# Performance work log

Measured on AMD Instinct MI355X. Metric: run time of the kernel, lower is better.

Reference implementation:

```python
import jax, jax.numpy as jnp
import numpy as np

N = 512    # nnodes
H = 8      # attention heads
C = 32     # gnn_repr_size (per head)
ER = 32    # edge_repr_size
FE = 3     # feat_emb_size
E = 16384  # edges (avg degree 32)


def gat_conv(x, edge_index, edge_attr, W, att_src, att_dst, We, att_edge, b):
    """PyG GATConv (edge_dim=1, concat=True, add_self_loops=True, eval mode)."""
    n = x.shape[0]
    h_, c_ = att_src.shape
    row, col = edge_index[0], edge_index[1]
    # self loops with fill_value='mean': mean of incoming edge_attr per target node
    deg = jax.ops.segment_sum(jnp.ones_like(edge_attr), col, num_segments=n)
    loop_attr = jax.ops.segment_sum(edge_attr, col, num_segments=n) / jnp.maximum(deg, 1.0)
    ar = jnp.arange(n)
    row = jnp.concatenate([row, ar])
    col = jnp.concatenate([col, ar])
    ea = jnp.concatenate([edge_attr, loop_attr])
    # node projections [n, H, C]
    h = (x @ W.T).reshape(n, h_, c_)
    a_src = jnp.sum(h * att_src, axis=-1)  # [n, H]
    a_dst = jnp.sum(h * att_dst, axis=-1)  # [n, H]
    e = (ea[:, None] @ We.T).reshape(-1, h_, c_)  # [E', H, C]
    a_e = jnp.sum(e * att_edge, axis=-1)          # [E', H]
    alpha = jax.nn.leaky_relu(a_src[row] + a_dst[col] + a_e, 0.2)
    # softmax over edges grouped by destination node
    amax = jax.ops.segment_max(alpha, col, num_segments=n)
    ex = jnp.exp(alpha - amax[col])
    denom = jax.ops.segment_sum(ex, col, num_segments=n)
    alpha = ex / (denom[col] + 1e-16)
    out = jax.ops.segment_sum(h[row] * alpha[..., None], col, num_segments=n)
    return out.reshape(n, h_ * c_) + b


def setup_inputs():
    key = jax.random.key(0)
    ks = jax.random.split(key, 24)
    s = 0.05
    HC = H * C
    in_len = N * ER + 3 * N + 3 * FE  # combiner1 input length
    return {
        "dist": jax.random.uniform(ks[0], (N, N), dtype=jnp.float32),
        "markov": jax.random.uniform(ks[1], (N, N), dtype=jnp.float32),
        "demand": jax.random.normal(ks[2], (N,), dtype=jnp.float32),
        "W_week": jax.random.normal(ks[3], (7, FE)) * s,
        "W_cap": jax.random.normal(ks[4], (26, FE)) * s,
        "W_veh": jax.random.normal(ks[5], (15, FE)) * s,
        "g1_W": jax.random.normal(ks[6], (HC, 1)) * s,
        "g1_att_src": jax.random.normal(ks[7], (H, C)) * s,
        "g1_att_dst": jax.random.normal(ks[8], (H, C)) * s,
        "g1_We": jax.random.normal(ks[9], (HC, 1)) * s,
        "g1_att_edge": jax.random.normal(ks[10], (H, C)) * s,
        "g1_b": jnp.zeros((HC,), dtype=jnp.float32),
        "g2_W": jax.random.normal(ks[11], (HC, HC)) * s,
        "g2_att_src": jax.random.normal(ks[12], (H, C)) * s,
        "g2_att_dst": jax.random.normal(ks[13], (H, C)) * s,
        "g2_We": jax.random.normal(ks[14], (HC, 1)) * s,
        "g2_att_edge": jax.random.normal(ks[15], (H, C)) * s,
        "g2_b": jnp.zeros((HC,), dtype=jnp.float32),
        "Wes": jax.random.normal(ks[16], (ER, 2 * HC)) * s,
        "bes": jnp.zeros((ER,), dtype=jnp.float32),
        "Wc1": jax.random.normal(ks[17], (N, in_len)) * 0.01,
        "bc1": jnp.zeros((N,), dtype=jnp.float32),
        "Wc2": jax.random.normal(ks[18], (N, N)) * s,
        "bc2": jnp.zeros((N,), dtype=jnp.float32),
        "stops": jax.random.randint(ks[19], (256,), 0, N),
        "edge_index": jax.random.randint(ks[20], (2, E), 0, N),
        "weekday": 3,
        "vehicles": 7,
        "capacity": 12,
    }


def reference(dist, markov, demand, W_week, W_cap, W_veh,
              g1_W, g1_att_src, g1_att_dst, g1_We, g1_att_edge, g1_b,
              g2_W, g2_att_src, g2_att_dst, g2_We, g2_att_edge, g2_b,
              Wes, bes, Wc1, bc1, Wc2, bc2,
              stops, edge_index, weekday, vehicles, capacity):
    n = dist.shape[0]
    dist = (dist - dist.min()) / (dist.max() - dist.min())
    x = demand[:, None]  # [n, 1]
    ea = markov[edge_index[0], edge_index[1]]  # [E]
    x = jax.nn.relu(gat_conv(x, edge_index, ea, g1_W, g1_att_src, g1_att_dst, g1_We, g1_att_edge, g1_b))
    x = jax.nn.relu(gat_conv(x, edge_index, ea, g2_W, g2_att_src, g2_att_dst, g2_We, g2_att_edge, g2_b))
    HC_ = x.shape[1]
    # all-pairs edge representation: concat(x[i], x[j]) over meshgrid -> [n*n, 2*HC]
    er = jnp.concatenate([
        jnp.broadcast_to(x[:, None, :], (n, n, HC_)),
        jnp.broadcast_to(x[None, :, :], (n, n, HC_)),
    ], axis=-1).reshape(n * n, 2 * HC_)
    er = (er @ Wes.T + bes).reshape(n, -1)  # [n, n*ER]
    week = jnp.broadcast_to(W_week[weekday], (n, W_week.shape[1]))
    cap = jnp.broadcast_to(W_cap[capacity], (n, W_cap.shape[1]))
    veh = jnp.broadcast_to(W_veh[vehicles], (n, W_veh.shape[1]))
    stop = jnp.broadcast_to(jnp.zeros((n,), dtype=dist.dtype).at[stops].set(1.0)[None, :], (n, n))
    feat = jnp.concatenate([er, dist, markov, week, cap, veh, stop], axis=1)
    out = jax.nn.relu(feat @ Wc1.T + bc1) @ Wc2.T + bc2
    return out
```

## Files before the change

kernel.cpp:

```cpp
#include <hip/hip_runtime.h>
#include <hip/hip_bf16.h>

typedef __hip_bfloat16 bf16;
typedef __attribute__((ext_vector_type(8))) short bf16x8;
typedef __attribute__((ext_vector_type(4))) float f32x4;

#define NNODE 512
#define NEDGE 16384
#define INLEN 17929
#define K1P   1088

#define WS_EA      0
#define WS_CSRC    16384
#define WS_CEA     32768
#define WS_DEG     49152
#define WS_STARTS  49664
#define WS_LATTR   50176
#define WS_MM      50688
#define WS_MMP     50690
#define WS_STOPV   50818
#define WS_AE      51330
#define WS_PS      51346
#define WS_G2WT    186624
#define WS_Y       317696
#define WS_ASRC    448768
#define WS_ADST    452864
#define WS_UV      456960
#define WS_K       489728
#define WS_APACK   490240
#define WS_BPACK   768768
#define WS_X1      1047296
#define WS_WC2B    1178368
#define WS_WESF    1309440
#define WS_ASRC2   1325824
#define WS_ADST2   1329920
#define WS_CURSOR  1334016
#define WS_DEGP    1334528
#define WS_LSUMP   1367296
#define WS_OUT1F   1400064

static __device__ __forceinline__ unsigned short f2bfbits(float x){
  bf16 b = __float2bfloat16(x);
  union { bf16 b; unsigned short u; } c; c.b = b; return c.u;
}

__global__ __launch_bounds__(256)
void k_prep(const float* __restrict__ demand, const float* __restrict__ W1,
            const float* __restrict__ att_s, const float* __restrict__ att_d,
            const int* __restrict__ stops, const float* __restrict__ Wes,
            const float* __restrict__ dist, const float* __restrict__ markov,
            const int* __restrict__ eidx,
            const float* __restrict__ g1We, const float* __restrict__ g1ae,
            const float* __restrict__ g2We, const float* __restrict__ g2ae,
            const float* __restrict__ g2W,  const float* __restrict__ g2as,
            const float* __restrict__ g2ad, const float* __restrict__ Wc2,
            float* __restrict__ outp, float* ws){
  int b = blockIdx.x, tid = threadIdx.x;
  if (b < 512){
    int hd = tid>>5, c = tid&31;
    float hv = demand[b] * W1[tid];
    float ps = hv * att_s[tid];
    float pd = hv * att_d[tid];
    for (int off=16; off; off>>=1){ ps += __shfl_down(ps,off,32); pd += __shfl_down(pd,off,32); }
    if (c==0){ ws[WS_ASRC + b*8+hd]=ps; ws[WS_ADST + b*8+hd]=pd; }
  } else if (b == 512){
    ws[WS_STOPV+tid] = 0.f; ws[WS_STOPV+256+tid] = 0.f;
    __syncthreads();
    ws[WS_STOPV + stops[tid]] = 1.0f;
    if (tid < 8){
      float s=0.f; for (int c=0;c<32;c++) s += g1We[tid*32+c]*g1ae[tid*32+c];
      ws[WS_AE+tid]=s;
    } else if (tid < 16){
      int h=tid-8; float s=0.f; for (int c=0;c<32;c++) s += g2We[h*32+c]*g2ae[h*32+c];
      ws[WS_AE+8+h]=s;
    }
  } else if (b < 515){
    for (int idx = (b-513)*8192 + tid; idx < (b-512)*8192; idx += 256){
      int k = idx>>8, c = idx&255;
      ws[WS_WESF+idx] = (k<32) ? Wes[k*512+c] : Wes[(k-32)*512+256+c];
    }
  } else if (b < 579){
    __shared__ float smn[256], smx[256];
    int p = b-515;
    float mn = 3.4e38f, mx = -3.4e38f;
    const float4* dv = (const float4*)(dist + p*4096);
    #pragma unroll
    for (int k=0;k<4;k++){
      float4 v = dv[k*256 + tid];
      mn = fminf(mn, fminf(fminf(v.x,v.y), fminf(v.z,v.w)));
      mx = fmaxf(mx, fmaxf(fmaxf(v.x,v.y), fmaxf(v.z,v.w)));
    }
    smn[tid]=mn; smx[tid]=mx; __syncthreads();
    for (int off=128; off; off>>=1){
      if (tid<off){ smn[tid]=fminf(smn[tid],smn[tid+off]); smx[tid]=fmaxf(smx[tid],smx[tid+off]); }
      __syncthreads();
    }
    if (tid==0){ ws[WS_MMP+p]=smn[0]; ws[WS_MMP+64+p]=smx[0]; }
  } else if (b < 643){
    __shared__ int   hd_[512];
    __shared__ float hf_[512];
    int k = b-579;
    hd_[tid]=0; hd_[256+tid]=0; hf_[tid]=0.f; hf_[256+tid]=0.f;
    __syncthreads();
    int e = k*256 + tid;
    int r = eidx[e], c = eidx[NEDGE+e];
    float a = markov[r*NNODE + c];
    ws[WS_EA+e] = a;
    atomicAdd(&hd_[c], 1);
    atomicAdd(&hf_[c], a);
    __syncthreads();
    ((int*)(ws+WS_DEGP))[k*512+tid]     = hd_[tid];
    ((int*)(ws+WS_DEGP))[k*512+256+tid] = hd_[256+tid];
    ws[WS_LSUMP + k*512+tid]     = hf_[tid];
    ws[WS_LSUMP + k*512+256+tid] = hf_[256+tid];
  } else if (b < 659){
    int j = b-643;
    const float* att = (j<8) ? g2as : g2ad;
    int h = j&7;
    float s = 0.f;
    for (int c=0;c<32;c++) s += att[h*32+c] * g2W[(h*32+c)*256 + tid];
    ws[WS_PS + j*256 + tid] = s;
  } else if (b < 675){
    __shared__ float T[64][65];
    int tb = b-659, tr = tb>>2, tc = tb&3;
    int w = tid>>6, c = tid&63;
    for (int k=0;k<16;k++){
      int r = k*4 + w;
      T[r][c] = g2W[(tr*64+r)*256 + tc*64 + c];
    }
    __syncthreads();
    for (int k=0;k<16;k++){
      int r = k*4 + w;
      ws[WS_G2WT + (tc*64+r)*256 + tr*64 + c] = T[c][r];
    }
  } else if (b == 675){
    ((int*)(ws+WS_CURSOR))[tid] = 0;
    ((int*)(ws+WS_CURSOR))[256+tid] = 0;
  } else if (b < 740){
    int blk = b - 676;
    const float4* src = (const float4*)(Wc2 + blk*4096);
    ushort4* dst = (ushort4*)((unsigned short*)(ws+WS_WC2B) + blk*4096);
    #pragma unroll
    for (int i=0;i<4;i++){
      float4 v = src[i*256+tid];
      ushort4 u;
      u.x = f2bfbits(v.x); u.y = f2bfbits(v.y);
      u.z = f2bfbits(v.z); u.w = f2bfbits(v.w);
      dst[i*256+tid] = u;
    }
  } else {
    int blk = b - 740;
    float4 z = {0.f,0.f,0.f,0.f};
    float4* o1f = (float4*)(ws + WS_OUT1F);
    float4* op  = (float4*)outp;
    o1f[blk*512 + tid] = z;
    o1f[blk*512 + 256 + tid] = z;
    op[blk*512 + tid] = z;
    op[blk*512 + 256 + tid] = z;
  }
}

__global__ __launch_bounds__(512)
void k_scansc(const int* __restrict__ eidx, float* ws){
  __shared__ int startS[512];
  __shared__ int wsum[8];
  int t = threadIdx.x, b = blockIdx.x, lane = t&63, w = t>>6;
  const int* dp = (const int*)(ws+WS_DEGP);
  int d = 0;
  #pragma unroll 8
  for (int k=0;k<64;k++) d += dp[k*512+t];
  int v = d;
  for (int off=1; off<64; off<<=1){
    int u = __shfl_up(v, off, 64);
    if (lane >= off) v += u;
  }
  if (lane==63) wsum[w] = v;
  __syncthreads();
  int base = 0;
  for (int k=0;k<w;k++) base += wsum[k];
  int incl = base + v;
  startS[t] = incl - d;
  if (b == 0){
    float l = 0.f;
    for (int k=0;k<64;k++) l += ws[WS_LSUMP+k*512+t];
    ((int*)(ws+WS_STARTS))[t] = incl - d;
    ((int*)(ws+WS_DEG))[t] = d;
    ws[WS_LATTR+t] = l / (float)(d>1 ? d : 1);
    if (t < 64){
      float mn = ws[WS_MMP+t], mx = ws[WS_MMP+64+t];
      for (int off=32; off; off>>=1){
        mn = fminf(mn, __shfl_down(mn,off,64));
        mx = fmaxf(mx, __shfl_down(mx,off,64));
      }
      if (t==0){ ws[WS_MM]=mn; ws[WS_MM+1]=mx; }
    }
  }
  __syncthreads();
  int e = b*512 + t;
  int c = eidx[NEDGE+e];
  int p = startS[c] + atomicAdd((int*)(ws+WS_CURSOR)+c, 1);
  ((int*)(ws+WS_CSRC))[p] = eidx[e];
  ws[WS_CEA+p] = ws[WS_EA+e];
}

template<int MODE>
__global__ __launch_bounds__(256)
void k_agg(const float* __restrict__ asrc, const float* __restrict__ adst,
           const float* __restrict__ AEp, const float* __restrict__ demand,
           const float* __restrict__ w1, const float* __restrict__ b1,
           float* ws){
  int t = blockIdx.x, tid = threadIdx.x, hd = tid>>5;
  __shared__ int   srcE[256];
  __shared__ float eaE[256];
  __shared__ float demE[256];
  __shared__ float Lall[256*8];
  __shared__ float AE[8], mh[8], dh[8], sw[8], sagg[8];
  __shared__ float xrow[256];
  if (tid<8) AE[tid]=AEp[tid];
  __syncthreads();
  const int* csrc = (const int*)(ws+WS_CSRC);
  const float* cea = ws+WS_CEA;
  int d  = ((const int*)(ws+WS_DEG))[t];
  int s0 = ((const int*)(ws+WS_STARTS))[t];
  if (d > 256) d = 256;
  for (int e=tid; e<d; e+=256){
    int s = csrc[s0+e];
    srcE[e]=s; eaE[e]=cea[s0+e];
    if (MODE==1) demE[e]=demand[s];
  }
  __syncthreads();
  {
    int h8 = tid&7;
    float adt = adst[t*8+h8], aeh = AE[h8];
    for (int e = tid>>3; e < d; e += 32){
      float a = asrc[srcE[e]*8+h8] + adt + eaE[e]*aeh;
      Lall[e*8+h8] = a>=0.f ? a : 0.2f*a;
    }
  }
  __syncthreads();
  {
    int h = tid>>5, j = tid&31;
    float aself = asrc[t*8+h] + adst[t*8+h] + ws[WS_LATTR+t]*AE[h];
    aself = aself>=0.f ? aself : 0.2f*aself;
    float mm = aself;
    for (int e=j; e<d; e+=32) mm = fmaxf(mm, Lall[e*8+h]);
    for (int off=16; off; off>>=1) mm = fmaxf(mm, __shfl_down(mm,off,32));
    mm = __shfl(mm, 0, 32);
    float dd = 0.f;
    for (int e=j; e<d; e+=32) dd += __expf(Lall[e*8+h]-mm);
    for (int off=16; off; off>>=1) dd += __shfl_down(dd,off,32);
    if (j==0){
      float se = __expf(aself-mm);
      mh[h]=mm; dh[h]=dd+se+1e-16f; sw[h]=se;
    }
  }
  __syncthreads();
  {
    int h8 = tid&7;
    for (int e = tid>>3; e < d; e += 32)
      Lall[e*8+h8] = __expf(Lall[e*8+h8] - mh[h8]);
  }
  __syncthreads();
  if (MODE == 1){
    int h = tid>>5, j = tid&31;
    float s = 0.f;
    for (int e=j; e<d; e+=32) s += Lall[e*8+h]*demE[e];
    for (int off=16; off; off>>=1) s += __shfl_down(s,off,32);
    if (j==0) sagg[h] = (s + sw[h]*demand[t]) / dh[h];
    __syncthreads();
    float v = fmaxf(sagg[hd]*w1[tid] + b1[tid], 0.f);
    xrow[tid] = v;
    ws[WS_X1 + t*256 + tid] = v;
    __syncthreads();
    if (tid < 64){
      int j2 = tid>>2, q = tid&3;
      const float* pr = ws + WS_PS + j2*256 + q*64;
      const float* xr = xrow + q*64;
      float p = 0.f;
      for (int c=0;c<64;c++) p += xr[c]*pr[c];
      p += __shfl_down(p,2,4);
      p += __shfl_down(p,1,4);
      if (q==0){
        if (j2<8) ws[WS_ASRC2 + t*8+j2] = p;
        else      ws[WS_ADST2 + t*8+(j2-8)] = p;
      }
    }
  } else {
    const float* x1 = ws + WS_X1;
    float a0 = sw[hd]*x1[t*256+tid], a1=0.f, a2=0.f, a3=0.f, a4=0.f, a5=0.f, a6=0.f, a7=0.f;
    int e = 0;
    for (; e+8<=d; e+=8){
      a0 += Lall[(e+0)*8+hd]*x1[srcE[e+0]*256+tid];
      a1 += Lall[(e+1)*8+hd]*x1[srcE[e+1]*256+tid];
      a2 += Lall[(e+2)*8+hd]*x1[srcE[e+2]*256+tid];
      a3 += Lall[(e+3)*8+hd]*x1[srcE[e+3]*256+tid];
      a4 += Lall[(e+4)*8+hd]*x1[srcE[e+4]*256+tid];
      a5 += Lall[(e+5)*8+hd]*x1[srcE[e+5]*256+tid];
      a6 += Lall[(e+6)*8+hd]*x1[srcE[e+6]*256+tid];
      a7 += Lall[(e+7)*8+hd]*x1[srcE[e+7]*256+tid];
    }
    for (; e<d; e++) a0 += Lall[e*8+hd]*x1[srcE[e]*256+tid];
    ws[WS_Y + t*256 + tid] = (((a0+a1)+(a2+a3))+((a4+a5)+(a6+a7)))/dh[hd];
  }
}

__global__ __launch_bounds__(256)
void k_post(const float* __restrict__ dist, const float* __restrict__ markov,
            const float* __restrict__ g2b, float* ws){
  __shared__ float yls[4][256];
  __shared__ float o2[4][256];
  __shared__ float uvs[4][64];
  int b = blockIdx.x, tid = threadIdx.x, n0 = b*4;
  #pragma unroll
  for (int n=0;n<4;n++) yls[n][tid] = ws[WS_Y + (n0+n)*256 + tid];
  __syncthreads();
  const float* T = ws + WS_G2WT;
  float a0=0.f,a1=0.f,a2=0.f,a3=0.f;
  #pragma unroll 4
  for (int c=0;c<256;c++){
    float w = T[c*256+tid];
    a0 += yls[0][c]*w; a1 += yls[1][c]*w;
    a2 += yls[2][c]*w; a3 += yls[3][c]*w;
  }
  float bb = g2b[tid];
  o2[0][tid]=fmaxf(a0+bb,0.f); o2[1][tid]=fmaxf(a1+bb,0.f);
  o2[2][tid]=fmaxf(a2+bb,0.f); o2[3][tid]=fmaxf(a3+bb,0.f);
  __syncthreads();
  {
    int n = tid>>6, k = tid&63;
    const float* wk = ws + WS_WESF + k*256;
    float p = 0.f;
    #pragma unroll 4
    for (int c=0;c<256;c++) p += o2[n][c]*wk[c];
    uvs[n][k] = p;
    ws[WS_UV + (n0+n)*64 + k] = p;
  }
  __syncthreads();
  float mn = ws[WS_MM], mx = ws[WS_MM+1];
  float inv = 1.0f/(mx-mn);
  bf16* ap = (bf16*)(ws+WS_APACK);
  #pragma unroll
  for (int n=0;n<4;n++){
    int t = n0+n;
    const float* drow = dist + t*512;
    const float* mrow = markov + t*512;
    for (int j=tid; j<K1P; j+=256){
      float v2;
      if (j<32)        v2 = uvs[n][j];
      else if (j<544)  v2 = (drow[j-32] - mn) * inv;
      else if (j<1056) v2 = mrow[j-544];
      else             v2 = 0.f;
      ap[(size_t)t*K1P + j] = __float2bfloat16(v2);
    }
  }
}

__global__ __launch_bounds__(1024)
void k_skpack(const float* __restrict__ Wc1, const float* __restrict__ bc1,
              const float* __restrict__ bes, const float* __restrict__ Wweek,
              const float* __restrict__ Wcap, const float* __restrict__ Wveh,
              const int* __restrict__ wd, const int* __restrict__ vh,
              const int* __restrict__ cp, float* ws){
  int o = blockIdx.x, tid = threadIdx.x;
  __shared__ float besf[32];
  __shared__ float red[512];
  __shared__ float red2[16];
  if (tid<32) besf[tid] = bes[tid];
  __syncthreads();
  const float* wr = Wc1 + (size_t)o*INLEN;
  bf16* bp  = (bf16*)(ws+WS_BPACK);
  float be = besf[tid&31];
  const float* uvp = ws + WS_UV + ((tid>>5)<<6) + 32 + (tid&31);
  float sP = 0.f, tP0=0.f, tP1=0.f, tP2=0.f, tP3=0.f;
  #pragma unroll
  for (int i=0;i<16;i+=4){
    float w0 = wr[tid + 1024*(i+0)];
    float w1 = wr[tid + 1024*(i+1)];
    float w2 = wr[tid + 1024*(i+2)];
    float w3 = wr[tid + 1024*(i+3)];
    float u0 = uvp[2048*(i+0)];
    float u1 = uvp[2048*(i+1)];
    float u2 = uvp[2048*(i+2)];
    float u3 = uvp[2048*(i+3)];
    sP += (w0+w1)+(w2+w3);
    tP0 += w0*(u0+be);
    tP1 += w1*(u1+be);
    tP2 += w2*(u2+be);
    tP3 += w3*(u3+be);
  }
  float tP = (tP0+tP1)+(tP2+tP3);
  if (tid < 512) tP += ws[WS_STOPV+tid] * wr[17417+tid];
  if (tid < 9){
    int g = tid/3, f = tid-g*3;
    float sv = (g==0) ? Wweek[wd[0]*3+f]
             : (g==1) ? Wcap[cp[0]*3+f]
                      : Wveh[vh[0]*3+f];
    tP += sv * wr[17408+tid];
  }
  int lane = tid&63, w = tid>>6;
  sP += __shfl_down(sP, 32, 64);
  if (lane < 32) red[w*32 + lane] = sP;
  for (int off=32; off; off>>=1) tP += __shfl_down(tP, off, 64);
  if (lane == 0) red2[w] = tP;
  __syncthreads();
  if (tid < 32){
    float s = 0.f;
    #pragma unroll
    for (int k=0;k<16;k++) s += red[k*32+tid];
    bp[(size_t)o*K1P + tid] = __float2bfloat16(s);
    bp[(size_t)o*K1P + 1056 + tid] = __float2bfloat16(0.f);
  } else if (tid == 32){
    float s = 0.f;
    #pragma unroll
    for (int k=0;k<16;k++) s += red2[k];
    ws[WS_K+o] = s + bc1[o];
  }
  bp[(size_t)o*K1P + 32 + tid] = __float2bfloat16(wr[16384+tid]);
}

__global__ __launch_bounds__(512)
void gemm1_splitk(const bf16* __restrict__ A, const bf16* __restrict__ B,
                  float* __restrict__ C, int N, int K){
  __shared__ short Als[2][4096];
  __shared__ short Bls[2][4096];
  const int tid = threadIdx.x;
  const int bm = blockIdx.y*64, bn = blockIdx.x*64;
  const int kz = blockIdx.z, NS = gridDim.z;
  const int nkT = K>>6;
  const int kb = (nkT*kz)/NS, ke = (nkT*(kz+1))/NS, cnt = ke-kb;
  const int wave = tid>>6, lane = tid&63;
  const int wm = wave>>2, wn = wave&3;
  const int r = lane&15, q = lane>>4;
  f32x4 acc[2] = {};
  const int lrow = tid>>3, lk8 = tid&7;
  const bf16* Ag = A + (size_t)(bm+lrow)*K + kb*64 + lk8*8;
  const bf16* Bg = B + (size_t)(bn+lrow)*K + kb*64 + lk8*8;
  const int sidx = ((lk8>>2)*256 + (lk8&3)*64 + lrow)*8;
  float4 av = *(const float4*)(Ag);
  float4 bv = *(const float4*)(Bg);
  *(float4*)(&Als[0][sidx]) = av;
  *(float4*)(&Bls[0][sidx]) = bv;
  __syncthreads();
  for (int kk=0; kk<cnt; kk++){
    int cur = kk&1, nxt = cur^1;
    if (kk+1 < cnt){
      av = *(const float4*)(Ag + (kk+1)*64);
      bv = *(const float4*)(Bg + (kk+1)*64);
    }
    #pragma unroll
    for (int k2=0; k2<2; k2++){
      bf16x8 bfr = *(const bf16x8*)(&Bls[cur][(k2*256 + q*64 + wn*16 + r)*8]);
      #pragma unroll
      for (int i=0;i<2;i++){
        bf16x8 af = *(const bf16x8*)(&Als[cur][(k2*256 + q*64 + wm*32 + i*16 + r)*8]);
        acc[i] = __builtin_amdgcn_mfma_f32_16x16x32_bf16(af, bfr, acc[i], 0,0,0);
      }
    }
    if (kk+1 < cnt){
      __syncthreads();
      *(float4*)(&Als[nxt][sidx]) = av;
      *(float4*)(&Bls[nxt][sidx]) = bv;
      __syncthreads();
    }
  }
  const int col = bn + wn*16 + r;
  #pragma unroll
  for (int i=0;i<2;i++){
    int row = bm + wm*32 + i*16 + q*4;
    #pragma unroll
    for (int g=0; g<4; g++)
      atomicAdd(&C[(size_t)(row+g)*N + col], acc[i][g]);
  }
}

__global__ __launch_bounds__(512)
void gemm2_f32a(const float* __restrict__ Af, const bf16* __restrict__ B,
                const float* __restrict__ kbias, const float* __restrict__ bc2,
                float* __restrict__ C){
  const int N = 512, K = 512;
  __shared__ short Als[2][4096];
  __shared__ short Bls[2][4096];
  const int tid = threadIdx.x;
  const int bm = blockIdx.y*64, bn = blockIdx.x*64;
  const int kz = blockIdx.z, NS = gridDim.z;
  const int nkT = K>>6;
  const int kb = (nkT*kz)/NS, ke = (nkT*(kz+1))/NS, cnt = ke-kb;
  const int wave = tid>>6, lane = tid&63;
  const int wm = wave>>2, wn = wave&3;
  const int r = lane&15, q = lane>>4;
  f32x4 acc[2] = {};
  const int lrow = tid>>3, lk8 = tid&7;
  const float* Ag = Af + (size_t)(bm+lrow)*K + kb*64 + lk8*8;
  const bf16*  Bg = B  + (size_t)(bn+lrow)*K + kb*64 + lk8*8;
  const float* Kg = kbias + kb*64 + lk8*8;
  const int sidx = ((lk8>>2)*256 + (lk8&3)*64 + lrow)*8;
  union PK { ushort u[8]; float4 f; };
  float4 x0, x1, k0, k1, bv;
  auto loadA = [&](int kk){
    x0 = *(const float4*)(Ag + kk*64);
    x1 = *(const float4*)(Ag + kk*64 + 4);
    k0 = *(const float4*)(Kg + kk*64);
    k1 = *(const float4*)(Kg + kk*64 + 4);
  };
  auto packA = [&]()->float4 {
    PK p;
    p.u[0]=f2bfbits(fmaxf(x0.x+k0.x,0.f));
    p.u[1]=f2bfbits(fmaxf(x0.y+k0.y,0.f));
    p.u[2]=f2bfbits(fmaxf(x0.z+k0.z,0.f));
    p.u[3]=f2bfbits(fmaxf(x0.w+k0.w,0.f));
    p.u[4]=f2bfbits(fmaxf(x1.x+k1.x,0.f));
    p.u[5]=f2bfbits(fmaxf(x1.y+k1.y,0.f));
    p.u[6]=f2bfbits(fmaxf(x1.z+k1.z,0.f));
    p.u[7]=f2bfbits(fmaxf(x1.w+k1.w,0.f));
    return p.f;
  };
  loadA(0);
  bv = *(const float4*)(Bg);
  *(float4*)(&Als[0][sidx]) = packA();
  *(float4*)(&Bls[0][sidx]) = bv;
  __syncthreads();
  for (int kk=0; kk<cnt; kk++){
    int cur = kk&1, nxt = cur^1;
    if (kk+1 < cnt){
      loadA(kk+1);
      bv = *(const float4*)(Bg + (kk+1)*64);
    }
    #pragma unroll
    for (int k2=0; k2<2; k2++){
      bf16x8 bfr = *(const bf16x8*)(&Bls[cur][(k2*256 + q*64 + wn*16 + r)*8]);
      #pragma unroll
      for (int i=0;i<2;i++){
        bf16x8 af = *(const bf16x8*)(&Als[cur][(k2*256 + q*64 + wm*32 + i*16 + r)*8]);
        acc[i] = __builtin_amdgcn_mfma_f32_16x16x32_bf16(af, bfr, acc[i], 0,0,0);
      }
    }
    if (kk+1 < cnt){
      __syncthreads();
      *(float4*)(&Als[nxt][sidx]) = packA();
      *(float4*)(&Bls[nxt][sidx]) = bv;
      __syncthreads();
    }
  }
  const int col = bn + wn*16 + r;
  const float bi = (kz==0) ? bc2[col] : 0.f;
  #pragma unroll
  for (int i=0;i<2;i++){
    int row = bm + wm*32 + i*16 + q*4;
    #pragma unroll
    for (int g=0; g<4; g++)
      atomicAdd(&C[(size_t)(row+g)*N + col], acc[i][g] + bi);
  }
}

extern "C" void kernel_launch(void* const* d_in, const int* in_sizes, int n_in,
                              void* d_out, int out_size, void* d_ws, size_t ws_size,
                              hipStream_t stream){
  const float* dist   = (const float*)d_in[0];
  const float* markov = (const float*)d_in[1];
  const float* demand = (const float*)d_in[2];
  const float* Wweek  = (const float*)d_in[3];
  const float* Wcap   = (const float*)d_in[4];
  const float* Wveh   = (const float*)d_in[5];
  const float* g1W    = (const float*)d_in[6];
  const float* g1as   = (const float*)d_in[7];
  const float* g1ad   = (const float*)d_in[8];
  const float* g1We   = (const float*)d_in[9];
  const float* g1ae   = (const float*)d_in[10];
  const float* g1b    = (const float*)d_in[11];
  const float* g2W    = (const float*)d_in[12];
  const float* g2as   = (const float*)d_in[13];
  const float* g2ad   = (const float*)d_in[14];
  const float* g2We   = (const float*)d_in[15];
  const float* g2ae   = (const float*)d_in[16];
  const float* g2b    = (const float*)d_in[17];
  const float* Wes    = (const float*)d_in[18];
  const float* bes    = (const float*)d_in[19];
  const float* Wc1    = (const float*)d_in[20];
  const float* bc1    = (const float*)d_in[21];
  const float* Wc2    = (const float*)d_in[22];
  const float* bc2    = (const float*)d_in[23];
  const int*   stops  = (const int*)d_in[24];
  const int*   eidx   = (const int*)d_in[25];
  const int*   wd     = (const int*)d_in[26];
  const int*   vh     = (const int*)d_in[27];
  const int*   cp     = (const int*)d_in[28];
  float* out = (float*)d_out;
  float* ws = (float*)d_ws;

  k_prep<<<868,256,0,stream>>>(demand, g1W, g1as, g1ad, stops, Wes, dist, markov, eidx,
                               g1We, g1ae, g2We, g2ae, g2W, g2as, g2ad, Wc2, out, ws);
  k_scansc<<<32,512,0,stream>>>(eidx, ws);
  k_agg<1><<<512,256,0,stream>>>(ws+WS_ASRC, ws+WS_ADST, ws+WS_AE, demand, g1W, g1b, ws);
  k_agg<2><<<512,256,0,stream>>>(ws+WS_ASRC2, ws+WS_ADST2, ws+WS_AE+8, demand, g1W, g1b, ws);
  k_post<<<128,256,0,stream>>>(dist, markov, g2b, ws);
  k_skpack<<<512,1024,0,stream>>>(Wc1, bc1, bes, Wweek, Wcap, Wveh, wd, vh, cp, ws);
  gemm1_splitk<<<dim3(8,8,4),512,0,stream>>>((const bf16*)(ws+WS_APACK), (const bf16*)(ws+WS_BPACK),
                                             ws+WS_OUT1F, 512, K1P);
  gemm2_f32a<<<dim3(8,8,2),512,0,stream>>>(ws+WS_OUT1F, (const bf16*)(ws+WS_WC2B),
                                           ws+WS_K, bc2, out);
}
```

Baseline: 214.7 us.

## Fuse GAT layer-2 projection and post-processing into aggregation kernels

Layer-2's linear projection moves ahead of aggregation: it is computed per node inside the first aggregation kernel (x1·W2ᵀ), so the second aggregation gathers already-projected features. The second aggregation then applies bias and ReLU, computes the edge-repr U/V projection, and packs the GEMM A rows, which removes the separate k_post kernel and the X1/Y round-trips. The transposed g2W and the Wes weights are stored as packed bf16 pairs to halve weight reads, at some cost in precision.

New measurement: 191.4 us. 1.12x faster.

```diff
diff --git a/kernel.cpp b/kernel.cpp
--- a/kernel.cpp
+++ b/kernel.cpp
@@ -22,14 +22,13 @@
 #define WS_AE      51330
 #define WS_PS      51346
 #define WS_G2WT    186624
-#define WS_Y       317696
+#define WS_H2      317696
 #define WS_ASRC    448768
 #define WS_ADST    452864
 #define WS_UV      456960
 #define WS_K       489728
 #define WS_APACK   490240
 #define WS_BPACK   768768
-#define WS_X1      1047296
 #define WS_WC2B    1178368
 #define WS_WESF    1309440
 #define WS_ASRC2   1325824
@@ -75,9 +74,16 @@
       ws[WS_AE+8+h]=s;
     }
   } else if (b < 515){
-    for (int idx = (b-513)*8192 + tid; idx < (b-512)*8192; idx += 256){
-      int k = idx>>8, c = idx&255;
-      ws[WS_WESF+idx] = (k<32) ? Wes[k*512+c] : Wes[(k-32)*512+256+c];
+    unsigned int* wp = (unsigned int*)(ws+WS_WESF);
+    int k0 = (b-513)*32;
+    for (int it=0; it<16; ++it){
+      int idx = it*256 + tid;
+      int k = k0 + (idx>>7), c2 = idx&127;
+      int c = 2*c2;
+      float lo, hi;
+      if (k<32){ lo = Wes[k*512+c];           hi = Wes[k*512+c+1]; }
+      else     { lo = Wes[(k-32)*512+256+c];  hi = Wes[(k-32)*512+256+c+1]; }
+      wp[k*128+c2] = ((unsigned int)f2bfbits(lo)) | (((unsigned int)f2bfbits(hi))<<16);
     }
   } else if (b < 579){
     __shared__ float smn[256], smx[256];
@@ -129,9 +135,13 @@
       T[r][c] = g2W[(tr*64+r)*256 + tc*64 + c];
     }
     __syncthreads();
-    for (int k=0;k<16;k++){
-      int r = k*4 + w;
-      ws[WS_G2WT + (tc*64+r)*256 + tr*64 + c] = T[c][r];
+    unsigned int* gp = (unsigned int*)(ws+WS_G2WT);
+    for (int k=0;k<8;k++){
+      int r0 = k*8 + w*2;
+      float lo = T[c][r0], hi = T[c][r0+1];
+      unsigned int u = ((unsigned int)f2bfbits(lo)) | (((unsigned int)f2bfbits(hi))<<16);
+      int i0 = tc*64 + r0;
+      gp[(i0>>1)*256 + tr*64 + c] = u;
     }
   } else if (b == 675){
     ((int*)(ws+WS_CURSOR))[tid] = 0;
@@ -205,9 +215,11 @@
 
 template<int MODE>
 __global__ __launch_bounds__(256)
-void k_agg(const float* __restrict__ asrc, const float* __restrict__ adst,
-           const float* __restrict__ AEp, const float* __restrict__ demand,
-           const float* __restrict__ w1, const float* __restrict__ b1,
+void k_agg(const float* __restrict__ hbuf, const float* __restrict__ asrc,
+           const float* __restrict__ adst, const float* __restrict__ AEp,
+           const float* __restrict__ bvec, const float* __restrict__ demand,
+           const float* __restrict__ w1,
+           const float* __restrict__ dist, const float* __restrict__ markov,
            float* ws){
   int t = blockIdx.x, tid = threadIdx.x, hd = tid>>5;
   __shared__ int   srcE[256];
@@ -215,7 +227,7 @@
   __shared__ float demE[256];
   __shared__ float Lall[256*8];
   __shared__ float AE[8], mh[8], dh[8], sw[8], sagg[8];
-  __shared__ float xrow[256];
+  __shared__ float xrow[256], uvrow[64];
   if (tid<8) AE[tid]=AEp[tid];
   __syncthreads();
   const int* csrc = (const int*)(ws+WS_CSRC);
@@ -268,10 +280,18 @@
     for (int off=16; off; off>>=1) s += __shfl_down(s,off,32);
     if (j==0) sagg[h] = (s + sw[h]*demand[t]) / dh[h];
     __syncthreads();
-    float v = fmaxf(sagg[hd]*w1[tid] + b1[tid], 0.f);
+    float v = fmaxf(sagg[hd]*w1[tid] + bvec[tid], 0.f);
     xrow[tid] = v;
-    ws[WS_X1 + t*256 + tid] = v;
-    __syncthreads();
+    __syncthreads();
+    const unsigned int* g2 = (const unsigned int*)(ws+WS_G2WT);
+    float h0=0.f, h1=0.f;
+    #pragma unroll 4
+    for (int p=0;p<128;p++){
+      unsigned int wv = g2[p*256+tid];
+      h0 += xrow[2*p]   * __uint_as_float(wv<<16);
+      h1 += xrow[2*p+1] * __uint_as_float(wv & 0xffff0000u);
+    }
+    ws[WS_H2 + t*256 + tid] = h0+h1;
     if (tid < 64){
       int j2 = tid>>2, q = tid&3;
       const float* pr = ws + WS_PS + j2*256 + q*64;
@@ -286,68 +306,45 @@
       }
     }
   } else {
-    const float* x1 = ws + WS_X1;
-    float a0 = sw[hd]*x1[t*256+tid], a1=0.f, a2=0.f, a3=0.f, a4=0.f, a5=0.f, a6=0.f, a7=0.f;
+    float a0 = sw[hd]*hbuf[t*256+tid], a1=0.f, a2=0.f, a3=0.f, a4=0.f, a5=0.f, a6=0.f, a7=0.f;
     int e = 0;
     for (; e+8<=d; e+=8){
-      a0 += Lall[(e+0)*8+hd]*x1[srcE[e+0]*256+tid];
-      a1 += Lall[(e+1)*8+hd]*x1[srcE[e+1]*256+tid];
-      a2 += Lall[(e+2)*8+hd]*x1[srcE[e+2]*256+tid];
-      a3 += Lall[(e+3)*8+hd]*x1[srcE[e+3]*256+tid];
-      a4 += Lall[(e+4)*8+hd]*x1[srcE[e+4]*256+tid];
-      a5 += Lall[(e+5)*8+hd]*x1[srcE[e+5]*256+tid];
-      a6 += Lall[(e+6)*8+hd]*x1[srcE[e+6]*256+tid];
-      a7 += Lall[(e+7)*8+hd]*x1[srcE[e+7]*256+tid];
-    }
-    for (; e<d; e++) a0 += Lall[e*8+hd]*x1[srcE[e]*256+tid];
-    ws[WS_Y + t*256 + tid] = (((a0+a1)+(a2+a3))+((a4+a5)+(a6+a7)))/dh[hd];
-  }
-}
-
-__global__ __launch_bounds__(256)
-void k_post(const float* __restrict__ dist, const float* __restrict__ markov,
-            const float* __restrict__ g2b, float* ws){
-  __shared__ float yls[4][256];
-  __shared__ float o2[4][256];
-  __shared__ float uvs[4][64];
-  int b = blockIdx.x, tid = threadIdx.x, n0 = b*4;
-  #pragma unroll
-  for (int n=0;n<4;n++) yls[n][tid] = ws[WS_Y + (n0+n)*256 + tid];
-  __syncthreads();
-  const float* T = ws + WS_G2WT;
-  float a0=0.f,a1=0.f,a2=0.f,a3=0.f;
-  #pragma unroll 4
-  for (int c=0;c<256;c++){
-    float w = T[c*256+tid];
-    a0 += yls[0][c]*w; a1 += yls[1][c]*w;
-    a2 += yls[2][c]*w; a3 += yls[3][c]*w;
-  }
-  float bb = g2b[tid];
-  o2[0][tid]=fmaxf(a0+bb,0.f); o2[1][tid]=fmaxf(a1+bb,0.f);
-  o2[2][tid]=fmaxf(a2+bb,0.f); o2[3][tid]=fmaxf(a3+bb,0.f);
-  __syncthreads();
-  {
-    int n = tid>>6, k = tid&63;
-    const float* wk = ws + WS_WESF + k*256;
-    float p = 0.f;
-    #pragma unroll 4
-    for (int c=0;c<256;c++) p += o2[n][c]*wk[c];
-    uvs[n][k] = p;
-    ws[WS_UV + (n0+n)*64 + k] = p;
-  }
-  __syncthreads();
-  float mn = ws[WS_MM], mx = ws[WS_MM+1];
-  float inv = 1.0f/(mx-mn);
-  bf16* ap = (bf16*)(ws+WS_APACK);
-  #pragma unroll
-  for (int n=0;n<4;n++){
-    int t = n0+n;
-    const float* drow = dist + t*512;
+      a0 += Lall[(e+0)*8+hd]*hbuf[srcE[e+0]*256+tid];
+      a1 += Lall[(e+1)*8+hd]*hbuf[srcE[e+1]*256+tid];
+      a2 += Lall[(e+2)*8+hd]*hbuf[srcE[e+2]*256+tid];
+      a3 += Lall[(e+3)*8+hd]*hbuf[srcE[e+3]*256+tid];
+      a4 += Lall[(e+4)*8+hd]*hbuf[srcE[e+4]*256+tid];
+      a5 += Lall[(e+5)*8+hd]*hbuf[srcE[e+5]*256+tid];
+      a6 += Lall[(e+6)*8+hd]*hbuf[srcE[e+6]*256+tid];
+      a7 += Lall[(e+7)*8+hd]*hbuf[srcE[e+7]*256+tid];
+    }
+    for (; e<d; e++) a0 += Lall[e*8+hd]*hbuf[srcE[e]*256+tid];
+    float v = fmaxf((((a0+a1)+(a2+a3))+((a4+a5)+(a6+a7)))/dh[hd] + bvec[tid], 0.f);
+    xrow[tid] = v;
+    __syncthreads();
+    int k = tid>>2, q = tid&3;
+    const unsigned int* wk = (const unsigned int*)(ws+WS_WESF) + k*128 + q*32;
+    const float* xr = xrow + q*64;
+    float p0=0.f, p1=0.f;
+    #pragma unroll 8
+    for (int c2=0;c2<32;c2++){
+      unsigned int wv = wk[c2];
+      p0 += xr[2*c2]   * __uint_as_float(wv<<16);
+      p1 += xr[2*c2+1] * __uint_as_float(wv & 0xffff0000u);
+    }
+    float p = p0+p1;
+    p += __shfl_down(p,2,4);
+    p += __shfl_down(p,1,4);
+    if (q==0){ ws[WS_UV + t*64+k] = p; uvrow[k] = p; }
+    __syncthreads();
+    float mn = ws[WS_MM], mx = ws[WS_MM+1];
+    float inv = 1.0f/(mx-mn);
+    bf16* ap = (bf16*)(ws+WS_APACK);
     const float* mrow = markov + t*512;
     for (int j=tid; j<K1P; j+=256){
       float v2;
-      if (j<32)        v2 = uvs[n][j];
-      else if (j<544)  v2 = (drow[j-32] - mn) * inv;
+      if (j<32)        v2 = uvrow[j];
+      else if (j<544)  v2 = (dist[t*512 + j-32] - mn) * inv;
       else if (j<1056) v2 = mrow[j-544];
       else             v2 = 0.f;
       ap[(size_t)t*K1P + j] = __float2bfloat16(v2);
@@ -590,9 +587,10 @@
   k_prep<<<868,256,0,stream>>>(demand, g1W, g1as, g1ad, stops, Wes, dist, markov, eidx,
                                g1We, g1ae, g2We, g2ae, g2W, g2as, g2ad, Wc2, out, ws);
   k_scansc<<<32,512,0,stream>>>(eidx, ws);
-  k_agg<1><<<512,256,0,stream>>>(ws+WS_ASRC, ws+WS_ADST, ws+WS_AE, demand, g1W, g1b, ws);
-  k_agg<2><<<512,256,0,stream>>>(ws+WS_ASRC2, ws+WS_ADST2, ws+WS_AE+8, demand, g1W, g1b, ws);
-  k_post<<<128,256,0,stream>>>(dist, markov, g2b, ws);
+  k_agg<1><<<512,256,0,stream>>>(nullptr, ws+WS_ASRC, ws+WS_ADST, ws+WS_AE, g1b,
+                                 demand, g1W, dist, markov, ws);
+  k_agg<2><<<512,256,0,stream>>>(ws+WS_H2, ws+WS_ASRC2, ws+WS_ADST2, ws+WS_AE+8, g2b,
+                                 demand, g1W, dist, markov, ws);
   k_skpack<<<512,1024,0,stream>>>(Wc1, bc1, bes, Wweek, Wcap, Wveh, wd, vh, cp, ws);
   gemm1_splitk<<<dim3(8,8,4),512,0,stream>>>((const bf16*)(ws+WS_APACK), (const bf16*)(ws+WS_BPACK),
                                              ws+WS_OUT1F, 512, K1P);
```
